# Performance work log

Hardware: AMD Instinct MI355X
Metric: run time of the kernel (lower is better)

## Reference

```python
import math
import jax, jax.numpy as jnp
import numpy as np

B, CH3, T = 64, 192, 2048  # B = batch*heads, CH3 = 3*head_dim

def setup_inputs() -> dict:
    key = jax.random.key(0)
    qkv = jax.random.normal(key, (B, CH3, T), dtype=jnp.float32)
    return {"qkv": qkv}

def reference(qkv):
    ch = qkv.shape[1] // 3
    q, k, v = jnp.split(qkv, 3, axis=1)  # each [B, ch, T]
    scale = 1.0 / math.sqrt(math.sqrt(ch))
    # scores [B, T(query), S(key)]
    weight = jnp.einsum('bct,bcs->bts', q * scale, k * scale)
    weight = jax.nn.softmax(weight.astype(jnp.float32), axis=-1).astype(weight.dtype)
    return jnp.einsum('bts,bcs->bct', weight, v)
```

## Files before the change

### kernel.cpp

```cpp
#include <hip/hip_runtime.h>


#define DHEAD 64
#define TLEN  2048
#define NB    64
#define BQ    256
#define BK    64
#define NT    (TLEN / BK)

typedef _Float16 h16x8 __attribute__((ext_vector_type(8)));
typedef _Float16 h16x2 __attribute__((ext_vector_type(2)));
typedef __fp16   fp16x2 __attribute__((ext_vector_type(2)));
typedef float    f32x16 __attribute__((ext_vector_type(16)));

#define QK_SCALE 0.42466090267246895f

extern "C" __device__ float __ocml_native_exp2_f32(float);

union H2U  { h16x2 h; fp16x2 f; unsigned u; };
union FRAG { h16x8 v; unsigned u[4]; };

__device__ __forceinline__ unsigned pk_u(float a, float b) {
    H2U x; x.f = __builtin_amdgcn_cvt_pkrtz(a, b); return x.u;
}

__device__ __forceinline__ int swz(int row, int col) {
    return row * 64 + (col ^ ((row & 7) << 3));
}
__device__ __forceinline__ int swzf(int c, int s) {
    return c * 64 + (s ^ (((c >> 3) & 7) << 2));
}

__global__ __launch_bounds__(256, 2)
void attn(const float* __restrict__ qkv, float* __restrict__ out) {
    __shared__ alignas(16) float    Kst[64 * 64];
    __shared__ alignas(16) _Float16 Ks[64 * 64];
    __shared__ alignas(16) _Float16 Vs[64 * 64];

    const int tid  = threadIdx.x;
    const int wave = tid >> 6;
    const int lane = tid & 63;
    const int h    = lane >> 5;
    const int c32  = lane & 31;

    const int flat = blockIdx.x + (int)gridDim.x * blockIdx.y;
    const int j8   = flat & 7, m8 = flat >> 3;
    const int b    = ((m8 & 7) << 3) | j8;
    const int t0   = (m8 >> 3) * BQ + wave * 64;

    const float* qg = qkv + ((size_t)b * 3 + 0) * DHEAD * TLEN;
    const float* kg = qkv + ((size_t)b * 3 + 1) * DHEAD * TLEN;
    const float* vg = qkv + ((size_t)b * 3 + 2) * DHEAD * TLEN;

    h16x8 qf[2][4];
    #pragma unroll
    for (int nb = 0; nb < 2; ++nb)
        #pragma unroll
        for (int kb = 0; kb < 4; ++kb) {
            const float* qp = qg + (size_t)(kb * 16 + h * 8) * TLEN + t0 + nb * 32 + c32;
            FRAG f;
            #pragma unroll
            for (int w = 0; w < 4; ++w)
                f.u[w] = pk_u(qp[(size_t)(2 * w) * TLEN] * QK_SCALE,
                              qp[(size_t)(2 * w + 1) * TLEN] * QK_SCALE);
            qf[nb][kb] = f.v;
        }

    f32x16 acco[2][2];
    #pragma unroll
    for (int cb = 0; cb < 2; ++cb)
        #pragma unroll
        for (int nb = 0; nb < 2; ++nb)
            #pragma unroll
            for (int r = 0; r < 16; ++r) acco[cb][nb][r] = 0.f;
    float lp[2] = {0.f, 0.f};

    const int sc = tid >> 2;
    const int sq = (tid & 3) * 16;
    const int ts_s   = tid >> 3;
    const int ts_c   = (tid & 7) * 8;
    const int ts_key = (tid & 7) << 2;

    float4 kc[4];
    h16x8  vc2[2];

    auto PREF = [&](int s0) {
        const float* kp = kg + (size_t)sc * TLEN + s0 + sq;
        const float* vp = vg + (size_t)sc * TLEN + s0 + sq;
        #pragma unroll
        for (int k = 0; k < 4; ++k) kc[k] = *(const float4*)(kp + 4 * k);
        float4 v0 = *(const float4*)(vp + 0);
        float4 v1 = *(const float4*)(vp + 4);
        float4 v2 = *(const float4*)(vp + 8);
        float4 v3 = *(const float4*)(vp + 12);
        FRAG a, c;
        a.u[0] = pk_u(v0.x, v0.y); a.u[1] = pk_u(v0.z, v0.w);
        a.u[2] = pk_u(v1.x, v1.y); a.u[3] = pk_u(v1.z, v1.w);
        c.u[0] = pk_u(v2.x, v2.y); c.u[1] = pk_u(v2.z, v2.w);
        c.u[2] = pk_u(v3.x, v3.y); c.u[3] = pk_u(v3.z, v3.w);
        vc2[0] = a.v; vc2[1] = c.v;
    };

    PREF(0);

    for (int it = 0; it < NT; ++it) {
        __syncthreads();
        #pragma unroll
        for (int k = 0; k < 4; ++k)
            *(float4*)&Kst[swzf(sc, sq + 4 * k)] = kc[k];
        *(h16x8*)&Vs[swz(sc, sq)]     = vc2[0];
        *(h16x8*)&Vs[swz(sc, sq + 8)] = vc2[1];
        __syncthreads();

        if (it + 1 < NT) PREF((it + 1) * BK);

        #pragma unroll
        for (int half = 0; half < 2; ++half) {
            const int s    = ts_s + half * 32;
            const int scol = s ^ ts_key;
            FRAG f;
            #pragma unroll
            for (int w = 0; w < 4; ++w) {
                float f0 = Kst[(ts_c + 2 * w) * 64 + scol];
                float f1 = Kst[(ts_c + 2 * w + 1) * 64 + scol];
                f.u[w] = pk_u(f0 * QK_SCALE, f1 * QK_SCALE);
            }
            *(h16x8*)&Ks[swz(s, ts_c)] = f.v;
        }
        __syncthreads();

        #pragma unroll
        for (int mb = 0; mb < 2; ++mb) {
            f32x16 accs[2];
            #pragma unroll
            for (int nb = 0; nb < 2; ++nb)
                #pragma unroll
                for (int r = 0; r < 16; ++r) accs[nb][r] = 0.f;

            __builtin_amdgcn_s_setprio(1);
            #pragma unroll
            for (int kb = 0; kb < 4; ++kb) {
                h16x8 ka = *(const h16x8*)&Ks[swz(mb * 32 + c32, kb * 16 + h * 8)];
                accs[0] = __builtin_amdgcn_mfma_f32_32x32x16_f16(ka, qf[0][kb], accs[0], 0, 0, 0);
                accs[1] = __builtin_amdgcn_mfma_f32_32x32x16_f16(ka, qf[1][kb], accs[1], 0, 0, 0);
            }
            __builtin_amdgcn_s_setprio(0);

            h16x8 pb[2][2];
            #pragma unroll
            for (int nb = 0; nb < 2; ++nb) {
                float e[16];
                #pragma unroll
                for (int r = 0; r < 16; ++r) e[r] = __ocml_native_exp2_f32(accs[nb][r]);
                float s0 = 0.f;
                #pragma unroll
                for (int r = 0; r < 16; ++r) s0 += e[r];
                lp[nb] += s0;
                #pragma unroll
                for (int kb16 = 0; kb16 < 2; ++kb16) {
                    const float* ee = e + kb16 * 8;
                    unsigned a01 = pk_u(ee[0], ee[1]);
                    unsigned a23 = pk_u(ee[2], ee[3]);
                    unsigned b01 = pk_u(ee[4], ee[5]);
                    unsigned b23 = pk_u(ee[6], ee[7]);
                    asm volatile("v_permlane32_swap_b32 %0, %1" : "+v"(a01), "+v"(b01));
                    asm volatile("v_permlane32_swap_b32 %0, %1" : "+v"(a23), "+v"(b23));
                    FRAG f;
                    f.u[0] = a01; f.u[1] = a23; f.u[2] = b01; f.u[3] = b23;
                    pb[kb16][nb] = f.v;
                }
            }

            __builtin_amdgcn_s_setprio(1);
            #pragma unroll
            for (int kb16 = 0; kb16 < 2; ++kb16) {
                const int scol = mb * 32 + kb16 * 16 + h * 8;
                #pragma unroll
                for (int cb = 0; cb < 2; ++cb) {
                    h16x8 va = *(const h16x8*)&Vs[swz(cb * 32 + c32, scol)];
                    acco[cb][0] = __builtin_amdgcn_mfma_f32_32x32x16_f16(va, pb[kb16][0], acco[cb][0], 0, 0, 0);
                    acco[cb][1] = __builtin_amdgcn_mfma_f32_32x32x16_f16(va, pb[kb16][1], acco[cb][1], 0, 0, 0);
                }
            }
            __builtin_amdgcn_s_setprio(0);
        }
    }

    float rinv[2];
    #pragma unroll
    for (int nb = 0; nb < 2; ++nb) {
        float l = lp[nb];
        l += __shfl_xor(l, 32);
        rinv[nb] = 1.0f / l;
    }

    float* ob = out + (size_t)b * DHEAD * TLEN + t0;
    #pragma unroll
    for (int cb = 0; cb < 2; ++cb)
        #pragma unroll
        for (int nb = 0; nb < 2; ++nb)
            #pragma unroll
            for (int r = 0; r < 16; ++r) {
                const int c = cb * 32 + (r & 3) + 8 * (r >> 2) + 4 * h;
                ob[(size_t)c * TLEN + nb * 32 + c32] = acco[cb][nb][r] * rinv[nb];
            }
}

extern "C" void kernel_launch(void* const* d_in, const int* in_sizes, int n_in,
                              void* d_out, int out_size, void* d_ws, size_t ws_size,
                              hipStream_t stream) {
    const float* qkv = (const float*)d_in[0];
    float* out = (float*)d_out;
    attn<<<dim3(TLEN / BQ, NB), 256, 0, stream>>>(qkv, out);
}
```

Measured before the change: 242.3 us.

## Pre-transpose and convert K to fp16 in a separate prep kernel

Adds a prep kernel that transposes K into a [T, D] fp16 layout with the scale already applied, writing it to workspace. The attention kernel then loads K fragments directly into the swizzled LDS tile. This removes the per-iteration fp32 staging buffer, the LDS transpose pass and one barrier per tile. The cost is an extra kernel launch plus one extra write and read of K in global memory.

```diff
diff --git a/kernel.cpp b/kernel.cpp
--- a/kernel.cpp
+++ b/kernel.cpp
@@ -7,6 +7,7 @@
 #define BQ    256
 #define BK    64
 #define NT    (TLEN / BK)
+#define LDT   65
 
 typedef _Float16 h16x8 __attribute__((ext_vector_type(8)));
 typedef _Float16 h16x2 __attribute__((ext_vector_type(2)));
@@ -27,13 +28,43 @@
 __device__ __forceinline__ int swz(int row, int col) {
     return row * 64 + (col ^ ((row & 7) << 3));
 }
-__device__ __forceinline__ int swzf(int c, int s) {
-    return c * 64 + (s ^ (((c >> 3) & 7) << 2));
+
+__global__ __launch_bounds__(256)
+void prep_k(const float* __restrict__ qkv, _Float16* __restrict__ ws) {
+    __shared__ float T32[64 * LDT];
+    const int tile = blockIdx.x, b = blockIdx.y;
+    const int tid = threadIdx.x;
+    const float* src = qkv + ((size_t)b * 3 + 1) * DHEAD * TLEN + tile * 64;
+    _Float16* dst = ws + (size_t)b * DHEAD * TLEN + (size_t)tile * 64 * DHEAD;
+    {
+        int c = tid >> 4, t4 = (tid & 15) * 4;
+        #pragma unroll
+        for (int rr = 0; rr < 4; ++rr, c += 16) {
+            float4 f = *(const float4*)(src + c * TLEN + t4);
+            T32[(t4 + 0) * LDT + c] = f.x;
+            T32[(t4 + 1) * LDT + c] = f.y;
+            T32[(t4 + 2) * LDT + c] = f.z;
+            T32[(t4 + 3) * LDT + c] = f.w;
+        }
+    }
+    __syncthreads();
+    #pragma unroll
+    for (int rep = 0; rep < 2; ++rep) {
+        int idx = rep * 256 + tid;
+        int t = idx >> 3, j = idx & 7;
+        const float* row = &T32[t * LDT + j * 8];
+        FRAG o;
+        o.u[0] = pk_u(row[0] * QK_SCALE, row[1] * QK_SCALE);
+        o.u[1] = pk_u(row[2] * QK_SCALE, row[3] * QK_SCALE);
+        o.u[2] = pk_u(row[4] * QK_SCALE, row[5] * QK_SCALE);
+        o.u[3] = pk_u(row[6] * QK_SCALE, row[7] * QK_SCALE);
+        *(h16x8*)(dst + t * DHEAD + j * 8) = o.v;
+    }
 }
 
 __global__ __launch_bounds__(256, 2)
-void attn(const float* __restrict__ qkv, float* __restrict__ out) {
-    __shared__ alignas(16) float    Kst[64 * 64];
+void attn(const float* __restrict__ qkv, const _Float16* __restrict__ kt,
+          float* __restrict__ out) {
     __shared__ alignas(16) _Float16 Ks[64 * 64];
     __shared__ alignas(16) _Float16 Vs[64 * 64];
 
@@ -49,21 +80,21 @@
     const int t0   = (m8 >> 3) * BQ + wave * 64;
 
     const float* qg = qkv + ((size_t)b * 3 + 0) * DHEAD * TLEN;
-    const float* kg = qkv + ((size_t)b * 3 + 1) * DHEAD * TLEN;
     const float* vg = qkv + ((size_t)b * 3 + 2) * DHEAD * TLEN;
+    const _Float16* kb = kt + (size_t)b * DHEAD * TLEN;
 
     h16x8 qf[2][4];
     #pragma unroll
     for (int nb = 0; nb < 2; ++nb)
         #pragma unroll
-        for (int kb = 0; kb < 4; ++kb) {
-            const float* qp = qg + (size_t)(kb * 16 + h * 8) * TLEN + t0 + nb * 32 + c32;
+        for (int kbq = 0; kbq < 4; ++kbq) {
+            const float* qp = qg + (size_t)(kbq * 16 + h * 8) * TLEN + t0 + nb * 32 + c32;
             FRAG f;
             #pragma unroll
             for (int w = 0; w < 4; ++w)
                 f.u[w] = pk_u(qp[(size_t)(2 * w) * TLEN] * QK_SCALE,
                               qp[(size_t)(2 * w + 1) * TLEN] * QK_SCALE);
-            qf[nb][kb] = f.v;
+            qf[nb][kbq] = f.v;
         }
 
     f32x16 acco[2][2];
@@ -75,20 +106,16 @@
             for (int r = 0; r < 16; ++r) acco[cb][nb][r] = 0.f;
     float lp[2] = {0.f, 0.f};
 
-    const int sc = tid >> 2;
+    const int sr = tid >> 2;
     const int sq = (tid & 3) * 16;
-    const int ts_s   = tid >> 3;
-    const int ts_c   = (tid & 7) * 8;
-    const int ts_key = (tid & 7) << 2;
-
-    float4 kc[4];
-    h16x8  vc2[2];
+
+    h16x8 kc2[2], vc2[2];
 
     auto PREF = [&](int s0) {
-        const float* kp = kg + (size_t)sc * TLEN + s0 + sq;
-        const float* vp = vg + (size_t)sc * TLEN + s0 + sq;
-        #pragma unroll
-        for (int k = 0; k < 4; ++k) kc[k] = *(const float4*)(kp + 4 * k);
+        const _Float16* kp = kb + (size_t)(s0 + sr) * DHEAD + sq;
+        kc2[0] = *(const h16x8*)(kp);
+        kc2[1] = *(const h16x8*)(kp + 8);
+        const float* vp = vg + (size_t)sr * TLEN + s0 + sq;
         float4 v0 = *(const float4*)(vp + 0);
         float4 v1 = *(const float4*)(vp + 4);
         float4 v2 = *(const float4*)(vp + 8);
@@ -105,29 +132,13 @@
 
     for (int it = 0; it < NT; ++it) {
         __syncthreads();
-        #pragma unroll
-        for (int k = 0; k < 4; ++k)
-            *(float4*)&Kst[swzf(sc, sq + 4 * k)] = kc[k];
-        *(h16x8*)&Vs[swz(sc, sq)]     = vc2[0];
-        *(h16x8*)&Vs[swz(sc, sq + 8)] = vc2[1];
+        *(h16x8*)&Ks[swz(sr, sq)]     = kc2[0];
+        *(h16x8*)&Ks[swz(sr, sq + 8)] = kc2[1];
+        *(h16x8*)&Vs[swz(sr, sq)]     = vc2[0];
+        *(h16x8*)&Vs[swz(sr, sq + 8)] = vc2[1];
         __syncthreads();
 
         if (it + 1 < NT) PREF((it + 1) * BK);
-
-        #pragma unroll
-        for (int half = 0; half < 2; ++half) {
-            const int s    = ts_s + half * 32;
-            const int scol = s ^ ts_key;
-            FRAG f;
-            #pragma unroll
-            for (int w = 0; w < 4; ++w) {
-                float f0 = Kst[(ts_c + 2 * w) * 64 + scol];
-                float f1 = Kst[(ts_c + 2 * w + 1) * 64 + scol];
-                f.u[w] = pk_u(f0 * QK_SCALE, f1 * QK_SCALE);
-            }
-            *(h16x8*)&Ks[swz(s, ts_c)] = f.v;
-        }
-        __syncthreads();
 
         #pragma unroll
         for (int mb = 0; mb < 2; ++mb) {
@@ -139,10 +150,10 @@
 
             __builtin_amdgcn_s_setprio(1);
             #pragma unroll
-            for (int kb = 0; kb < 4; ++kb) {
-                h16x8 ka = *(const h16x8*)&Ks[swz(mb * 32 + c32, kb * 16 + h * 8)];
-                accs[0] = __builtin_amdgcn_mfma_f32_32x32x16_f16(ka, qf[0][kb], accs[0], 0, 0, 0);
-                accs[1] = __builtin_amdgcn_mfma_f32_32x32x16_f16(ka, qf[1][kb], accs[1], 0, 0, 0);
+            for (int kbq = 0; kbq < 4; ++kbq) {
+                h16x8 ka = *(const h16x8*)&Ks[swz(mb * 32 + c32, kbq * 16 + h * 8)];
+                accs[0] = __builtin_amdgcn_mfma_f32_32x32x16_f16(ka, qf[0][kbq], accs[0], 0, 0, 0);
+                accs[1] = __builtin_amdgcn_mfma_f32_32x32x16_f16(ka, qf[1][kbq], accs[1], 0, 0, 0);
             }
             __builtin_amdgcn_s_setprio(0);
 
@@ -210,6 +221,8 @@
                               void* d_out, int out_size, void* d_ws, size_t ws_size,
                               hipStream_t stream) {
     const float* qkv = (const float*)d_in[0];
+    _Float16* ws = (_Float16*)d_ws;
     float* out = (float*)d_out;
-    attn<<<dim3(TLEN / BQ, NB), 256, 0, stream>>>(qkv, out);
-}
+    prep_k<<<dim3(TLEN / 64, NB), 256, 0, stream>>>(qkv, ws);
+    attn<<<dim3(TLEN / BQ, NB), 256, 0, stream>>>(qkv, ws, out);
+}
```

Measured after the change: 219.9 us. 1.1x faster.
